# Optimization experiments

Hardware: AMD Instinct MI355X
Metric: run time of the kernel (lower is better)

The kernel has to match this reference:

```python
import jax, jax.numpy as jnp
import numpy as np
import math

B, S, D, H, DFF, E, TOPK = 2, 2048, 768, 12, 3072, 8, 2
DH = D // H
EPS = 1e-5


def _ln(x, g, b):
    mu = jnp.mean(x, axis=-1, keepdims=True)
    var = jnp.mean(jnp.square(x - mu), axis=-1, keepdims=True)
    return (x - mu) * jax.lax.rsqrt(var + EPS) * g + b


def _router(x, rw, rb):
    # x: [B,S,D] -> probs [B,S,E], topk indices [B,S,K]
    logits = jnp.einsum('bsd,de->bse', x, rw) + rb
    probs = jax.nn.softmax(logits, axis=-1)
    topv, topi = jax.lax.top_k(probs, TOPK)
    return probs, topv, topi


def setup_inputs() -> dict:
    key = jax.random.key(0)
    ks = jax.random.split(key, 12)
    s = 0.02
    inp = {
        'x': jax.random.normal(ks[0], (B, S, D), dtype=jnp.float32),
        'wq': jax.random.normal(ks[1], (D, D), dtype=jnp.float32) * s,
        'bq': jnp.zeros((D,), jnp.float32),
        'wk': jax.random.normal(ks[2], (D, D), dtype=jnp.float32) * s,
        'bk': jnp.zeros((D,), jnp.float32),
        'wv': jax.random.normal(ks[3], (D, D), dtype=jnp.float32) * s,
        'bv': jnp.zeros((D,), jnp.float32),
        'wo': jax.random.normal(ks[4], (D, D), dtype=jnp.float32) * s,
        'bo': jnp.zeros((D,), jnp.float32),
        'norm1_g': jnp.ones((D,), jnp.float32),
        'norm1_b': jnp.zeros((D,), jnp.float32),
        'router_w': jax.random.normal(ks[5], (D, E), dtype=jnp.float32) * s,
        'router_b': jnp.zeros((E,), jnp.float32),
        'ew1': jax.random.normal(ks[6], (E, D, DFF), dtype=jnp.float32) * s,
        'eb1': jnp.zeros((E, DFF), jnp.float32),
        'ew2': jax.random.normal(ks[7], (E, DFF, D), dtype=jnp.float32) * s,
        'eb2': jnp.zeros((E, D), jnp.float32),
        'norm2_g': jnp.ones((D,), jnp.float32),
        'norm2_b': jnp.zeros((D,), jnp.float32),
    }
    return inp


def reference(x, wq, bq, wk, bk, wv, bv, wo, bo,
              norm1_g, norm1_b, router_w, router_b,
              ew1, eb1, ew2, eb2, norm2_g, norm2_b):
    # ---- multi-head self-attention ----
    def proj(w, b):
        return (jnp.einsum('bsd,de->bse', x, w) + b).reshape(B, S, H, DH).transpose(0, 2, 1, 3)
    q, k, v = proj(wq, bq), proj(wk, bk), proj(wv, bv)
    scores = jnp.einsum('bhqd,bhkd->bhqk', q, k) / math.sqrt(DH)
    attn = jax.nn.softmax(scores, axis=-1)
    ctx = jnp.einsum('bhqk,bhkd->bhqd', attn, v).transpose(0, 2, 1, 3).reshape(B, S, D)
    attn_out = jnp.einsum('bsd,de->bse', ctx, wo) + bo
    x1 = _ln(x + attn_out, norm1_g, norm1_b)

    # ---- MoE: top-k routing with renormalized gates ----
    probs, topv, topi = _router(x1, router_w, router_b)
    gates = topv / jnp.sum(topv, axis=-1, keepdims=True)          # [B,S,K]
    # combine weights per expert: [B,S,E]
    combine = jnp.sum(jax.nn.one_hot(topi, E, dtype=x1.dtype) * gates[..., None], axis=-2)
    moe_out = jnp.zeros_like(x1)
    for e in range(E):  # fixed small expert count
        h = jax.nn.relu(jnp.einsum('bsd,df->bsf', x1, ew1[e]) + eb1[e])
        y = jnp.einsum('bsf,fd->bsd', h, ew2[e]) + eb2[e]
        moe_out = moe_out + combine[..., e:e + 1] * y
    x2 = _ln(x1 + moe_out, norm2_g, norm2_b)

    # ---- redundant second router call + load-balancing aux loss ----
    probs2, _, topi2 = _router(x2, router_w, router_b)
    mask2 = jax.nn.one_hot(topi2, E, dtype=x2.dtype)              # [B,S,K,E]
    frac = jnp.mean(mask2, axis=(0, 1, 2))                        # fraction routed per expert
    prob = jnp.mean(probs2, axis=(0, 1))                          # mean router prob per expert
    aux_loss = E * jnp.sum(frac * prob)
    return (x2, aux_loss)
```

## Files before the change

kernel.cpp:

```cpp
#include <hip/hip_runtime.h>

typedef _Float16 f16;
typedef _Float16 f16x8 __attribute__((ext_vector_type(8)));
typedef _Float16 f16x4v __attribute__((ext_vector_type(4)));
typedef float f32x4 __attribute__((ext_vector_type(4)));

#define THREADS 256
#define BM 128
#define BN 128
#define BKK 64

#define WSCALE 256.0f
#define WDESCALE (1.0f/256.0f)

static __device__ __forceinline__ float wred_sum(float x){
#pragma unroll
  for (int o = 32; o; o >>= 1) x += __shfl_xor(x, o);
  return x;
}
static __device__ __forceinline__ int wred_sumi(int x){
#pragma unroll
  for (int o = 32; o; o >>= 1) x += __shfl_xor(x, o);
  return x;
}
static __device__ __forceinline__ float bred_sum(float x){
  __shared__ float r[4];
  x = wred_sum(x);
  if ((threadIdx.x & 63) == 0) r[threadIdx.x >> 6] = x;
  __syncthreads();
  float s = r[0] + r[1] + r[2] + r[3];
  __syncthreads();
  return s;
}

template<class Epi>
static __device__ __forceinline__ void gemm_core(const f16* A, const f16* BT,
                                                 int m0, int K, int N, int n0, Epi epi)
{
  __shared__ __align__(16) f16 Al[BM][BKK];
  __shared__ __align__(16) f16 Bl[BN][BKK];
  const int t = threadIdx.x;
  const int lane = t & 63, wave = t >> 6;
  const int wr = wave >> 1, wc = wave & 1;

  const f16* gA[4];
  const f16* gB[4];
#pragma unroll
  for (int i = 0; i < 4; ++i) {
    int c = i * THREADS + t;
    int r = c >> 3;
    int kc = (((c & 7) ^ (r & 7)) << 3);
    gA[i] = A + (size_t)(m0 + r) * K + kc;
    gB[i] = BT + (size_t)(n0 + r) * K + kc;
  }

  f32x4 acc[4][4];
#pragma unroll
  for (int i = 0; i < 4; ++i)
#pragma unroll
    for (int j = 0; j < 4; ++j)
#pragma unroll
      for (int r = 0; r < 4; ++r) acc[i][j][r] = 0.0f;

  f16* Als = &Al[0][0];
  f16* Bls = &Bl[0][0];

  for (int k0 = 0; k0 < K; k0 += BKK) {
    __syncthreads();
#pragma unroll
    for (int i = 0; i < 4; ++i) {
      int c = i * THREADS + t;
      __builtin_amdgcn_global_load_lds(
          (const __attribute__((address_space(1))) void*)(gA[i] + k0),
          (__attribute__((address_space(3))) void*)(Als + (size_t)c * 8), 16, 0, 0);
      __builtin_amdgcn_global_load_lds(
          (const __attribute__((address_space(1))) void*)(gB[i] + k0),
          (__attribute__((address_space(3))) void*)(Bls + (size_t)c * 8), 16, 0, 0);
    }
    __syncthreads();
#pragma unroll
    for (int kk = 0; kk < BKK; kk += 32) {
      const int lrow = lane & 15, lk = (lane >> 4) * 8;
      const int sx = (lrow & 7) << 3;
      f16x8 af[4], bf[4];
#pragma unroll
      for (int mf = 0; mf < 4; ++mf)
        af[mf] = *(const f16x8*)&Als[(size_t)(wr * 64 + mf * 16 + lrow) * BKK + ((kk + lk) ^ sx)];
#pragma unroll
      for (int nf = 0; nf < 4; ++nf)
        bf[nf] = *(const f16x8*)&Bls[(size_t)(wc * 64 + nf * 16 + lrow) * BKK + ((kk + lk) ^ sx)];
#pragma unroll
      for (int mf = 0; mf < 4; ++mf)
#pragma unroll
        for (int nf = 0; nf < 4; ++nf)
          acc[mf][nf] = __builtin_amdgcn_mfma_f32_16x16x32_f16(af[mf], bf[nf], acc[mf][nf], 0, 0, 0);
    }
  }
  const int lr4 = (lane >> 4) * 4, lc = lane & 15;
#pragma unroll
  for (int mf = 0; mf < 4; ++mf)
#pragma unroll
    for (int nf = 0; nf < 4; ++nf)
#pragma unroll
      for (int r = 0; r < 4; ++r) {
        int row = wr * 64 + mf * 16 + lr4 + r;
        int col = n0 + wc * 64 + nf * 16 + lc;
        epi(row, col, acc[mf][nf][r]);
      }
}

__global__ __launch_bounds__(256) void k_cvt(const float* x, f16* o){
  size_t i = (size_t)blockIdx.x * 256 + threadIdx.x;
  float4 v = ((const float4*)x)[i];
  f16x4v h;
  h[0] = (f16)v.x; h[1] = (f16)v.y; h[2] = (f16)v.z; h[3] = (f16)v.w;
  *(f16x4v*)(o + i * 4) = h;
}

__global__ __launch_bounds__(256) void k_transpose(const float* in, f16* out, int Kd, int Nd){
  __shared__ float tl[32][33];
  const float* ip = in + (size_t)blockIdx.z * Kd * Nd;
  f16* op = out + (size_t)blockIdx.z * Kd * Nd;
  int n0 = blockIdx.x * 32, k0 = blockIdx.y * 32;
  int tx = threadIdx.x & 31, ty = threadIdx.x >> 5;
#pragma unroll
  for (int j = 0; j < 32; j += 8) tl[ty + j][tx] = ip[(size_t)(k0 + ty + j) * Nd + n0 + tx];
  __syncthreads();
#pragma unroll
  for (int j = 0; j < 32; j += 8) op[(size_t)(n0 + ty + j) * Kd + k0 + tx] = (f16)(tl[tx][ty + j] * WSCALE);
}

__global__ __launch_bounds__(256) void k_gemm_qkv(const f16* xb,
    const f16* wqT, const f16* wkT, const f16* wvT,
    const float* bq, const float* bk, const float* bv,
    f16* Q, f16* Ko, f16* V)
{
  int m0 = blockIdx.x * 128, n0 = blockIdx.y * 128, z = blockIdx.z;
  const f16* BT = (z == 0) ? wqT : ((z == 1) ? wkT : wvT);
  const float* bias = (z == 0) ? bq : ((z == 1) ? bk : bv);
  auto epi = [&](int row, int col, float vv) {
    int grow = m0 + row;
    int b = grow >> 11, s = grow & 2047;
    int h = col >> 6, dh = col & 63;
    float val = vv * WDESCALE + bias[col];
    if (z == 2) V[(((size_t)b * 12 + h) * 64 + dh) * 2048 + s] = (f16)val;
    else ((z == 0) ? Q : Ko)[(((size_t)b * 12 + h) * 2048 + s) * 64 + dh] = (f16)val;
  };
  gemm_core(xb, BT, m0, 768, 768, n0, epi);
}

__global__ __launch_bounds__(256, 4) void k_fattn(const f16* Qf, const f16* Kf,
                                                  const f16* Vf, float* Opart, float* lpart)
{
  __shared__ __align__(16) f16 Kl[64][72];
  __shared__ __align__(16) f16 Vl[64][72];
  __shared__ __align__(16) f16 Pl[64][72];
  const int t = threadIdx.x, lane = t & 63, wid = t >> 6;
  const int lc = lane & 15, g = lane >> 4;
  const int q0 = blockIdx.x * 64, bh = blockIdx.y, sp = blockIdx.z;
  const f16* Qh = Qf + (size_t)bh * 2048 * 64;
  const f16* Kh = Kf + ((size_t)bh * 2048 + sp * 1024) * 64;
  const f16* Vh = Vf + (size_t)bh * 64 * 2048 + sp * 1024;

  const float C1 = 0.125f * 1.44269504f;
  const float C2 = 9.0f - 2.0f * 1.44269504f;

  f16x8 aq[2];
#pragma unroll
  for (int kk = 0; kk < 2; ++kk)
    aq[kk] = *(const f16x8*)(Qh + (size_t)(q0 + wid * 16 + lc) * 64 + kk * 32 + g * 8);

  f32x4 acco[4];
  float l_[4];
#pragma unroll
  for (int nf = 0; nf < 4; ++nf)
#pragma unroll
    for (int r = 0; r < 4; ++r) acco[nf][r] = 0.f;
#pragma unroll
  for (int r = 0; r < 4; ++r) l_[r] = 0.f;

  f16x8 sk[2], sv[2];
#pragma unroll
  for (int i = 0; i < 2; ++i) {
    int c = i * 256 + t;
    sk[i] = *(const f16x8*)(Kh + (size_t)(c >> 3) * 64 + (c & 7) * 8);
    sv[i] = *(const f16x8*)(Vh + (size_t)(c >> 3) * 2048 + (c & 7) * 8);
  }

  for (int j = 0; j < 16; ++j) {
    __syncthreads();
#pragma unroll
    for (int i = 0; i < 2; ++i) {
      int c = i * 256 + t;
      *(f16x8*)&Kl[c >> 3][(c & 7) * 8] = sk[i];
      *(f16x8*)&Vl[c >> 3][(c & 7) * 8] = sv[i];
    }
    __syncthreads();

    if (j < 15) {
      const int kv1 = (j + 1) * 64;
#pragma unroll
      for (int i = 0; i < 2; ++i) {
        int c = i * 256 + t;
        sk[i] = *(const f16x8*)(Kh + (size_t)(kv1 + (c >> 3)) * 64 + (c & 7) * 8);
        sv[i] = *(const f16x8*)(Vh + (size_t)(c >> 3) * 2048 + kv1 + (c & 7) * 8);
      }
    }

    f32x4 acc[4];
#pragma unroll
    for (int nf = 0; nf < 4; ++nf)
#pragma unroll
      for (int r = 0; r < 4; ++r) acc[nf][r] = 0.f;
#pragma unroll
    for (int kk = 0; kk < 2; ++kk) {
      f16x8 bk[4];
#pragma unroll
      for (int nf = 0; nf < 4; ++nf) bk[nf] = *(const f16x8*)&Kl[nf * 16 + lc][kk * 32 + g * 8];
#pragma unroll
      for (int nf = 0; nf < 4; ++nf)
        acc[nf] = __builtin_amdgcn_mfma_f32_16x16x32_f16(aq[kk], bk[nf], acc[nf], 0, 0, 0);
    }

    {
      const int prow = wid * 16 + g * 4;
#pragma unroll
      for (int r = 0; r < 4; ++r) {
        float ls = 0.f;
#pragma unroll
        for (int nf = 0; nf < 4; ++nf) {
          float p = exp2f(fmaf(acc[nf][r], C1, C2));
          Pl[prow + r][nf * 16 + lc] = (f16)p;
          ls += p;
        }
        l_[r] += ls;
      }
    }

#pragma unroll
    for (int kk = 0; kk < 2; ++kk) {
      f16x8 ap, bv[4];
      ap = *(const f16x8*)&Pl[wid * 16 + lc][kk * 32 + g * 8];
#pragma unroll
      for (int nf = 0; nf < 4; ++nf) bv[nf] = *(const f16x8*)&Vl[nf * 16 + lc][kk * 32 + g * 8];
#pragma unroll
      for (int nf = 0; nf < 4; ++nf)
        acco[nf] = __builtin_amdgcn_mfma_f32_16x16x32_f16(ap, bv[nf], acco[nf], 0, 0, 0);
    }
  }

  float* Op = Opart + ((size_t)(sp * 24 + bh) * 2048 + q0) * 64;
  float* lp = lpart + (size_t)(sp * 24 + bh) * 2048 + q0;
#pragma unroll
  for (int r = 0; r < 4; ++r) {
    float lr = l_[r];
#pragma unroll
    for (int o = 1; o < 16; o <<= 1) lr += __shfl_xor(lr, o);
    if (lc == 0) lp[wid * 16 + g * 4 + r] = lr;
#pragma unroll
    for (int nf = 0; nf < 4; ++nf)
      Op[(size_t)(wid * 16 + g * 4 + r) * 64 + nf * 16 + lc] = acco[nf][r];
  }
}

__global__ __launch_bounds__(256) void k_attcomb(const float* Opart, const float* lpart, f16* ctx){
  size_t base = ((size_t)blockIdx.x * 256 + threadIdx.x) * 4;
  size_t row = base >> 6; int dh = base & 63;
  int bh = (int)(row >> 11), qr = (int)(row & 2047);
  int b = bh / 12, h = bh - b * 12;
  const float4 o0 = *(const float4*)(Opart + base);
  const float4 o1 = *(const float4*)(Opart + base + (size_t)24 * 2048 * 64);
  float inv = 1.f / (lpart[row] + lpart[row + 24 * 2048]);
  f16x4v hv;
  hv[0] = (f16)((o0.x + o1.x) * inv);
  hv[1] = (f16)((o0.y + o1.y) * inv);
  hv[2] = (f16)((o0.z + o1.z) * inv);
  hv[3] = (f16)((o0.w + o1.w) * inv);
  *(f16x4v*)(ctx + ((size_t)b * 2048 + qr) * 768 + h * 64 + dh) = hv;
}

__global__ __launch_bounds__(256) void k_gemm_oproj(const f16* ctx, const f16* woT,
    const float* bo, const float* x, float* x1pre)
{
  int m0 = blockIdx.x * 128, n0 = blockIdx.y * 128;
  auto epi = [&](int row, int col, float vv) {
    size_t i = (size_t)(m0 + row) * 768 + col;
    x1pre[i] = x[i] + vv * WDESCALE + bo[col];
  };
  gemm_core(ctx, woT, m0, 768, 768, n0, epi);
}

__global__ __launch_bounds__(256) void k_ln(const float* in, const float* add,
    const float* g, const float* b, float* outf, f16* outh)
{
  size_t row = blockIdx.x;
  int t = threadIdx.x;
  const float* p = in + row * 768;
  float v[3];
  float s = 0.f;
#pragma unroll
  for (int i = 0; i < 3; ++i) {
    float xv = p[t + i * 256];
    if (add) xv += add[row * 768 + t + i * 256];
    v[i] = xv; s += xv;
  }
  float mu = bred_sum(s) * (1.f / 768.f);
  float q = 0.f;
#pragma unroll
  for (int i = 0; i < 3; ++i) { float d = v[i] - mu; q += d * d; }
  float var = bred_sum(q) * (1.f / 768.f);
  float inv = rsqrtf(var + 1e-5f);
#pragma unroll
  for (int i = 0; i < 3; ++i) {
    int c = t + i * 256;
    float y = (v[i] - mu) * inv * g[c] + b[c];
    outf[row * 768 + c] = y;
    if (outh) outh[row * 768 + c] = (f16)y;
  }
}

__global__ __launch_bounds__(256) void k_ln_moe(const float* x1, const f16* ys,
    const int* inv_map, const float* gates, const float* g, const float* b, float* outf)
{
  size_t row = blockIdx.x;
  int t = threadIdx.x;
  int sl0 = inv_map[row * 2], sl1 = inv_map[row * 2 + 1];
  float g0 = gates[row * 2], g1 = gates[row * 2 + 1];
  const float* p = x1 + row * 768;
  const f16* y0 = ys + (size_t)sl0 * 768;
  const f16* y1 = ys + (size_t)sl1 * 768;
  float v[3];
  float s = 0.f;
#pragma unroll
  for (int i = 0; i < 3; ++i) {
    int c = t + i * 256;
    float xv = p[c] + g0 * (float)y0[c] + g1 * (float)y1[c];
    v[i] = xv; s += xv;
  }
  float mu = bred_sum(s) * (1.f / 768.f);
  float q = 0.f;
#pragma unroll
  for (int i = 0; i < 3; ++i) { float d = v[i] - mu; q += d * d; }
  float var = bred_sum(q) * (1.f / 768.f);
  float inv = rsqrtf(var + 1e-5f);
#pragma unroll
  for (int i = 0; i < 3; ++i) {
    int c = t + i * 256;
    outf[row * 768 + c] = (v[i] - mu) * inv * g[c] + b[c];
  }
}

__global__ __launch_bounds__(256) void k_router(const float* X, const float* rw, const float* rb,
    int* topi, float* gates, float* pprob_part, int* pcnt_part, int mode)
{
  __shared__ float sp[4][8];
  __shared__ int   si[4][2];
  int wave = threadIdx.x >> 6;
  int tok = blockIdx.x * 4 + wave;
  int lane = threadIdx.x & 63;
  const float* xr = X + (size_t)tok * 768;
  float a0=0,a1=0,a2=0,a3=0,a4=0,a5=0,a6=0,a7=0;
#pragma unroll
  for (int i = 0; i < 12; ++i) {
    int d = lane + i * 64;
    float xv = xr[d];
    float4 w0 = *(const float4*)(rw + d * 8);
    float4 w1 = *(const float4*)(rw + d * 8 + 4);
    a0 += xv*w0.x; a1 += xv*w0.y; a2 += xv*w0.z; a3 += xv*w0.w;
    a4 += xv*w1.x; a5 += xv*w1.y; a6 += xv*w1.z; a7 += xv*w1.w;
  }
  a0=wred_sum(a0); a1=wred_sum(a1); a2=wred_sum(a2); a3=wred_sum(a3);
  a4=wred_sum(a4); a5=wred_sum(a5); a6=wred_sum(a6); a7=wred_sum(a7);
  if (lane == 0) {
    float lg[8] = {a0+rb[0],a1+rb[1],a2+rb[2],a3+rb[3],a4+rb[4],a5+rb[5],a6+rb[6],a7+rb[7]};
    float mx = lg[0];
    for (int e = 1; e < 8; ++e) mx = fmaxf(mx, lg[e]);
    float pp[8], ssum = 0.f;
    for (int e = 0; e < 8; ++e) { pp[e] = expf(lg[e] - mx); ssum += pp[e]; }
    float invs = 1.f / ssum;
    for (int e = 0; e < 8; ++e) pp[e] *= invs;
    int i1 = 0; float p1 = pp[0];
    for (int e = 1; e < 8; ++e) if (pp[e] > p1) { p1 = pp[e]; i1 = e; }
    int i2 = -1; float p2 = -1.f;
    for (int e = 0; e < 8; ++e) if (e != i1 && pp[e] > p2) { p2 = pp[e]; i2 = e; }
    if (mode == 1) {
      float gs = 1.f / (p1 + p2);
      topi[tok*2] = i1; topi[tok*2+1] = i2;
      gates[tok*2] = p1*gs; gates[tok*2+1] = p2*gs;
    } else {
      for (int e = 0; e < 8; ++e) sp[wave][e] = pp[e];
      si[wave][0] = i1; si[wave][1] = i2;
    }
  }
  if (mode == 2) {
    __syncthreads();
    int t = threadIdx.x;
    if (t < 8) {
      float s = sp[0][t] + sp[1][t] + sp[2][t] + sp[3][t];
      int c = 0;
#pragma unroll
      for (int w = 0; w < 4; ++w) c += (si[w][0] == t) + (si[w][1] == t);
      pprob_part[blockIdx.x * 8 + t] = s;
      pcnt_part[blockIdx.x * 8 + t] = c;
    }
  }
}

__global__ __launch_bounds__(256) void k_plan(const int* topi, int* offal,
    int* tile_e, int* tile_r0, int* tile_e2, int* tile_r02)
{
  __shared__ int hist[8];
  int t = threadIdx.x, lane = t & 63;
  if (t < 8) hist[t] = 0;
  __syncthreads();
  int loc[8] = {0,0,0,0,0,0,0,0};
  for (int i = t; i < 8192; i += 256) ++loc[topi[i]];
#pragma unroll
  for (int e = 0; e < 8; ++e) {
    int s = wred_sumi(loc[e]);
    if (lane == 0) atomicAdd(&hist[e], s);
  }
  __syncthreads();
  if (t == 0) {
    int off = 0, t1 = 0, t2 = 0;
    for (int e = 0; e < 8; ++e) {
      offal[e] = off;
      int nt = (hist[e] + 255) >> 8;
      for (int i = 0; i < nt; ++i) {
        tile_e[t1] = e; tile_r0[t1] = off + i * 256; ++t1;
        tile_e2[t2] = e; tile_r02[t2] = off + i * 256; ++t2;
        tile_e2[t2] = e; tile_r02[t2] = off + i * 256 + 128; ++t2;
      }
      off += nt << 8;
    }
    for (; t1 < 40; ++t1) { tile_e[t1] = -1; tile_r0[t1] = 0; }
    for (; t2 < 80; ++t2) { tile_e2[t2] = -1; tile_r02[t2] = 0; }
  }
}

__global__ __launch_bounds__(512) void k_scatter(const int* topi, const float* gates,
    const int* offal, int* perm, float* gate_s, int* inv_map)
{
  int w = threadIdx.x >> 6, lane = threadIdx.x & 63;
  int base = offal[w];
  for (int it = 0; it < 128; ++it) {
    int i = it * 64 + lane;
    int e = topi[i];
    bool act = (e == w);
    unsigned long long mask = __ballot(act);
    if (act) {
      int pos = base + __popcll(mask & ((1ull << lane) - 1ull));
      perm[pos] = i >> 1;
      gate_s[pos] = gates[i];
      inv_map[i] = pos;
    }
    base += __popcll(mask);
  }
}

__global__ __launch_bounds__(512, 1) void k_gemm_moe1(const f16* x1b, const f16* ew1T,
    const float* eb1, const int* tile_e, const int* tile_r0, const int* perm, f16* hbuf)
{
  __shared__ __align__(16) f16 Al[2][256][64];
  __shared__ __align__(16) f16 Bl[2][256][64];
  int e = tile_e[blockIdx.x];
  if (e < 0) return;
  int s0 = tile_r0[blockIdx.x];
  int n0 = blockIdx.y * 256;
  const f16* BT = ew1T + (size_t)e * 3072 * 768 + (size_t)n0 * 768;
  const float* be = eb1 + e * 3072;

  const int t = threadIdx.x;
  const int lane = t & 63, wave = t >> 6;
  const int wr = wave >> 2, wc = wave & 3;

  const f16* gA[4];
  const f16* gB[4];
#pragma unroll
  for (int i = 0; i < 4; ++i) {
    int c = i * 512 + t;
    int r = c >> 3;
    int kc = (((c & 7) ^ (r & 7)) << 3);
    gA[i] = x1b + (size_t)perm[s0 + r] * 768 + kc;
    gB[i] = BT + (size_t)r * 768 + kc;
  }

  f32x4 acc[8][4];
#pragma unroll
  for (int i = 0; i < 8; ++i)
#pragma unroll
    for (int j = 0; j < 4; ++j)
#pragma unroll
      for (int r = 0; r < 4; ++r) acc[i][j][r] = 0.0f;

  auto stage = [&](int buf, int k0) {
    f16* Ad = &Al[buf][0][0];
    f16* Bd = &Bl[buf][0][0];
#pragma unroll
    for (int i = 0; i < 4; ++i) {
      int c = i * 512 + t;
      __builtin_amdgcn_global_load_lds(
          (const __attribute__((address_space(1))) void*)(gA[i] + k0),
          (__attribute__((address_space(3))) void*)(Ad + (size_t)c * 8), 16, 0, 0);
      __builtin_amdgcn_global_load_lds(
          (const __attribute__((address_space(1))) void*)(gB[i] + k0),
          (__attribute__((address_space(3))) void*)(Bd + (size_t)c * 8), 16, 0, 0);
    }
  };

  stage(0, 0);
  stage(1, 64);

  for (int ks = 0; ks < 12; ++ks) {
    const int cur = ks & 1;
    if (ks < 11) asm volatile("s_waitcnt vmcnt(8)" ::: "memory");
    else         asm volatile("s_waitcnt vmcnt(0)" ::: "memory");
    __builtin_amdgcn_s_barrier();
    asm volatile("" ::: "memory");

    const f16* Ab = &Al[cur][0][0];
    const f16* Bb = &Bl[cur][0][0];
#pragma unroll
    for (int kk = 0; kk < 64; kk += 32) {
      const int lrow = lane & 15, lk = (lane >> 4) * 8;
      const int sx = (lrow & 7) << 3;
      f16x8 af[8], bf[4];
#pragma unroll
      for (int mf = 0; mf < 8; ++mf)
        af[mf] = *(const f16x8*)&Ab[(size_t)(wr * 128 + mf * 16 + lrow) * 64 + ((kk + lk) ^ sx)];
#pragma unroll
      for (int nf = 0; nf < 4; ++nf)
        bf[nf] = *(const f16x8*)&Bb[(size_t)(wc * 64 + nf * 16 + lrow) * 64 + ((kk + lk) ^ sx)];
#pragma unroll
      for (int mf = 0; mf < 8; ++mf)
#pragma unroll
        for (int nf = 0; nf < 4; ++nf)
          acc[mf][nf] = __builtin_amdgcn_mfma_f32_16x16x32_f16(af[mf], bf[nf], acc[mf][nf], 0, 0, 0);
    }

    asm volatile("" ::: "memory");
    __builtin_amdgcn_s_barrier();
    asm volatile("" ::: "memory");
    if (ks < 10) stage(cur, (ks + 2) * 64);
  }

  const int lr4 = (lane >> 4) * 4, lc = lane & 15;
#pragma unroll
  for (int mf = 0; mf < 8; ++mf)
#pragma unroll
    for (int nf = 0; nf < 4; ++nf)
#pragma unroll
      for (int r = 0; r < 4; ++r) {
        int row = wr * 128 + mf * 16 + lr4 + r;
        int col = n0 + wc * 64 + nf * 16 + lc;
        hbuf[(size_t)(s0 + row) * 3072 + col] = (f16)fmaxf(acc[mf][nf][r] * WDESCALE + be[col], 0.f);
      }
}

__global__ __launch_bounds__(256) void k_gemm_moe2(const f16* hbuf, const f16* ew2T,
    const float* eb2, const int* tile_e2, const int* tile_r02, f16* yslots)
{
  int e = tile_e2[blockIdx.x];
  if (e < 0) return;
  int s0 = tile_r02[blockIdx.x];
  int n0 = blockIdx.y * 128;
  const f16* A = hbuf + (size_t)s0 * 3072;
  const f16* BT = ew2T + (size_t)e * 768 * 3072;
  const float* be = eb2 + e * 768;
  auto epi = [&](int row, int col, float vv) {
    yslots[(size_t)(s0 + row) * 768 + col] = (f16)(vv * WDESCALE + be[col]);
  };
  gemm_core(A, BT, 0, 3072, 768, n0, epi);
}

__global__ __launch_bounds__(256) void k_final(const float* pprob, const int* pcnt, float* out){
  __shared__ float sp[256];
  __shared__ int sc[256];
  int t = threadIdx.x, e = t & 7, g = t >> 3;
  float s = 0.f; int c = 0;
  for (int b = g; b < 1024; b += 32) { s += pprob[b * 8 + e]; c += pcnt[b * 8 + e]; }
  sp[t] = s; sc[t] = c;
  __syncthreads();
  if (t < 8) {
    float ss = 0.f; int cc = 0;
    for (int g2 = 0; g2 < 32; ++g2) { ss += sp[t + g2 * 8]; cc += sc[t + g2 * 8]; }
    sp[t] = ss; sc[t] = cc;
  }
  __syncthreads();
  if (t == 0) {
    float a = 0.f;
    for (int e2 = 0; e2 < 8; ++e2)
      a += ((float)sc[e2] * (1.f / 8192.f)) * (sp[e2] * (1.f / 4096.f));
    out[(size_t)4096 * 768] = 8.f * a;
  }
}

extern "C" void kernel_launch(void* const* d_in, const int* in_sizes, int n_in,
                              void* d_out, int out_size, void* d_ws, size_t ws_size,
                              hipStream_t stream)
{
  const float* x   = (const float*)d_in[0];
  const float* wq  = (const float*)d_in[1];
  const float* bq  = (const float*)d_in[2];
  const float* wk  = (const float*)d_in[3];
  const float* bk  = (const float*)d_in[4];
  const float* wv  = (const float*)d_in[5];
  const float* bv  = (const float*)d_in[6];
  const float* wo  = (const float*)d_in[7];
  const float* bo  = (const float*)d_in[8];
  const float* n1g = (const float*)d_in[9];
  const float* n1b = (const float*)d_in[10];
  const float* rw  = (const float*)d_in[11];
  const float* rb  = (const float*)d_in[12];
  const float* ew1 = (const float*)d_in[13];
  const float* eb1 = (const float*)d_in[14];
  const float* ew2 = (const float*)d_in[15];
  const float* eb2 = (const float*)d_in[16];
  const float* n2g = (const float*)d_in[17];
  const float* n2b = (const float*)d_in[18];
  float* out = (float*)d_out;
  char* ws = (char*)d_ws;

  size_t oWQT,oWKT,oWVT,oWOT,oEW1T,oEW2T,oXB,oQ,oK,oV,oCTX,oX1,oX1B,oYS;
  size_t oTOPI,oGATES,oOFF,oTE,oTR,oTE2,oTR2,oPERM,oGS,oINV,oH,oPP,oPC,oOP,oLP;

  {
    size_t off = 0;
    auto al = [&](size_t bytes) { size_t o = off; off += (bytes + 255) & ~(size_t)255; return o; };
    oWQT = al((size_t)768*768*2); oWKT = al((size_t)768*768*2);
    oWVT = al((size_t)768*768*2); oWOT = al((size_t)768*768*2);
    oEW1T = al((size_t)8*768*3072*2); oEW2T = al((size_t)8*768*3072*2);
    oXB  = al((size_t)4096*768*2);
    oQ   = al((size_t)24*2048*64*2); oK = al((size_t)24*2048*64*2); oV = al((size_t)24*2048*64*2);
    oCTX = al((size_t)4096*768*2);
    oX1  = al((size_t)4096*768*4);
    oX1B = al((size_t)4096*768*2);
    oYS  = al((size_t)10240*768*2);
    oTOPI = al(4096*2*4); oGATES = al(4096*2*4);
    oOFF = al(256);
    oTE = al(256); oTR = al(256); oTE2 = al(512); oTR2 = al(512);
    oPERM = al(10240*4); oGS = al(10240*4); oINV = al(8192*4);
    oH = al((size_t)10240*3072*2);
    oPP = al(1024*8*4); oPC = al(1024*8*4);
    oOP = al((size_t)2*24*2048*64*4);
    oLP = al((size_t)2*24*2048*4);
    (void)ws_size;
  }

  f16* wqT  = (f16*)(ws + oWQT);
  f16* wkT  = (f16*)(ws + oWKT);
  f16* wvT  = (f16*)(ws + oWVT);
  f16* woT  = (f16*)(ws + oWOT);
  f16* ew1T = (f16*)(ws + oEW1T);
  f16* ew2T = (f16*)(ws + oEW2T);
  f16* xb   = (f16*)(ws + oXB);
  f16* Qf   = (f16*)(ws + oQ);
  f16* Kf   = (f16*)(ws + oK);
  f16* Vf   = (f16*)(ws + oV);
  f16* ctxb = (f16*)(ws + oCTX);
  float* x1 = (float*)(ws + oX1);
  f16* x1bb = (f16*)(ws + oX1B);
  f16* yslots = (f16*)(ws + oYS);
  int* topi = (int*)(ws + oTOPI);
  float* gates = (float*)(ws + oGATES);
  int* offal  = (int*)(ws + oOFF);
  int* tile_e = (int*)(ws + oTE);
  int* tile_r0= (int*)(ws + oTR);
  int* tile_e2 = (int*)(ws + oTE2);
  int* tile_r02= (int*)(ws + oTR2);
  int* perm   = (int*)(ws + oPERM);
  float* gate_s = (float*)(ws + oGS);
  int* inv_map = (int*)(ws + oINV);
  f16* hbuf   = (f16*)(ws + oH);
  float* pprob = (float*)(ws + oPP);
  int* pcnt   = (int*)(ws + oPC);
  float* Opart = (float*)(ws + oOP);
  float* lpart = (float*)(ws + oLP);

  (void)in_sizes; (void)n_in; (void)out_size;

  hipMemsetAsync(ws + oPERM, 0, 2 * 10240 * 4, stream);

  k_cvt<<<3072, 256, 0, stream>>>(x, xb);
  k_transpose<<<dim3(24,24,1), 256, 0, stream>>>(wq, wqT, 768, 768);
  k_transpose<<<dim3(24,24,1), 256, 0, stream>>>(wk, wkT, 768, 768);
  k_transpose<<<dim3(24,24,1), 256, 0, stream>>>(wv, wvT, 768, 768);
  k_transpose<<<dim3(24,24,1), 256, 0, stream>>>(wo, woT, 768, 768);
  k_transpose<<<dim3(96,24,8), 256, 0, stream>>>(ew1, ew1T, 768, 3072);
  k_transpose<<<dim3(24,96,8), 256, 0, stream>>>(ew2, ew2T, 3072, 768);

  k_gemm_qkv<<<dim3(32,6,3), 256, 0, stream>>>(xb, wqT, wkT, wvT, bq, bk, bv, Qf, Kf, Vf);
  k_fattn<<<dim3(32,24,2), 256, 0, stream>>>(Qf, Kf, Vf, Opart, lpart);
  k_attcomb<<<3072, 256, 0, stream>>>(Opart, lpart, ctxb);
  k_gemm_oproj<<<dim3(32,6), 256, 0, stream>>>(ctxb, woT, bo, x, x1);
  k_ln<<<4096, 256, 0, stream>>>(x1, nullptr, n1g, n1b, x1, x1bb);

  k_router<<<1024, 256, 0, stream>>>(x1, rw, rb, topi, gates, pprob, pcnt, 1);
  k_plan<<<1, 256, 0, stream>>>(topi, offal, tile_e, tile_r0, tile_e2, tile_r02);
  k_scatter<<<1, 512, 0, stream>>>(topi, gates, offal, perm, gate_s, inv_map);
  k_gemm_moe1<<<dim3(40,12), 512, 0, stream>>>(x1bb, ew1T, eb1, tile_e, tile_r0, perm, hbuf);
  k_gemm_moe2<<<dim3(80,6), 256, 0, stream>>>(hbuf, ew2T, eb2, tile_e2, tile_r02, yslots);

  k_ln_moe<<<4096, 256, 0, stream>>>(x1, yslots, inv_map, gates, n2g, n2b, out);
  k_router<<<1024, 256, 0, stream>>>(out, rw, rb, topi, gates, pprob, pcnt, 2);
  k_final<<<1, 256, 0, stream>>>(pprob, pcnt, out);
}
```

Before: 438.3 us.

## Rewrite MoE down-projection GEMM with 128x256 tiles and triple-buffered direct-to-LDS loads

```diff
diff --git a/kernel.cpp b/kernel.cpp
--- a/kernel.cpp
+++ b/kernel.cpp
@@ -557,20 +557,131 @@
       }
 }
 
-__global__ __launch_bounds__(256) void k_gemm_moe2(const f16* hbuf, const f16* ew2T,
+__global__ __launch_bounds__(512, 1) void k_gemm_moe2(const f16* hbuf, const f16* ew2T,
     const float* eb2, const int* tile_e2, const int* tile_r02, f16* yslots)
 {
+  __shared__ __align__(16) f16 Al[3][128][64];
+  __shared__ __align__(16) f16 Bl[3][256][64];
   int e = tile_e2[blockIdx.x];
   if (e < 0) return;
   int s0 = tile_r02[blockIdx.x];
-  int n0 = blockIdx.y * 128;
-  const f16* A = hbuf + (size_t)s0 * 3072;
-  const f16* BT = ew2T + (size_t)e * 768 * 3072;
+  int n0 = blockIdx.y * 256;
+  const f16* A  = hbuf + (size_t)s0 * 3072;
+  const f16* BT = ew2T + (size_t)e * 768 * 3072 + (size_t)n0 * 3072;
   const float* be = eb2 + e * 768;
-  auto epi = [&](int row, int col, float vv) {
-    yslots[(size_t)(s0 + row) * 768 + col] = (f16)(vv * WDESCALE + be[col]);
+
+  const int t = threadIdx.x;
+  const int lane = t & 63, wave = t >> 6;
+  const int wr = wave >> 2, wc = wave & 3;
+
+  const f16* gA[2];
+  const f16* gB[4];
+#pragma unroll
+  for (int i = 0; i < 2; ++i) {
+    int c = i * 512 + t;
+    int r = c >> 3;
+    int kc = (((c & 7) ^ (r & 7)) << 3);
+    gA[i] = A + (size_t)r * 3072 + kc;
+  }
+#pragma unroll
+  for (int i = 0; i < 4; ++i) {
+    int c = i * 512 + t;
+    int r = c >> 3;
+    int kc = (((c & 7) ^ (r & 7)) << 3);
+    gB[i] = BT + (size_t)r * 3072 + kc;
+  }
+
+  f32x4 acc[4][4];
+#pragma unroll
+  for (int i = 0; i < 4; ++i)
+#pragma unroll
+    for (int j = 0; j < 4; ++j)
+#pragma unroll
+      for (int r = 0; r < 4; ++r) acc[i][j][r] = 0.0f;
+
+  auto stage = [&](int buf, int k0) {
+    f16* Ad = &Al[buf][0][0];
+    f16* Bd = &Bl[buf][0][0];
+#pragma unroll
+    for (int i = 0; i < 2; ++i) {
+      int c = i * 512 + t;
+      __builtin_amdgcn_global_load_lds(
+          (const __attribute__((address_space(1))) void*)(gA[i] + k0),
+          (__attribute__((address_space(3))) void*)(Ad + (size_t)c * 8), 16, 0, 0);
+    }
+#pragma unroll
+    for (int i = 0; i < 4; ++i) {
+      int c = i * 512 + t;
+      __builtin_amdgcn_global_load_lds(
+          (const __attribute__((address_space(1))) void*)(gB[i] + k0),
+          (__attribute__((address_space(3))) void*)(Bd + (size_t)c * 8), 16, 0, 0);
+    }
   };
-  gemm_core(A, BT, 0, 3072, 768, n0, epi);
+
+  stage(0, 0);
+  stage(1, 64);
+
+  int bufc = 0;
+  for (int ks = 0; ks < 48; ++ks) {
+    if (ks < 47) asm volatile("s_waitcnt vmcnt(6)" ::: "memory");
+    else         asm volatile("s_waitcnt vmcnt(0)" ::: "memory");
+    __builtin_amdgcn_s_barrier();
+    asm volatile("" ::: "memory");
+
+    const f16* Ab = &Al[bufc][0][0];
+    const f16* Bb = &Bl[bufc][0][0];
+    const int lrow = lane & 15, lk = (lane >> 4) * 8;
+    const int sx = (lrow & 7) << 3;
+
+    {
+      f16x8 af[4], bf[4];
+#pragma unroll
+      for (int mf = 0; mf < 4; ++mf)
+        af[mf] = *(const f16x8*)&Ab[(size_t)(wr * 64 + mf * 16 + lrow) * 64 + ((0 + lk) ^ sx)];
+#pragma unroll
+      for (int nf = 0; nf < 4; ++nf)
+        bf[nf] = *(const f16x8*)&Bb[(size_t)(wc * 64 + nf * 16 + lrow) * 64 + ((0 + lk) ^ sx)];
+#pragma unroll
+      for (int mf = 0; mf < 4; ++mf)
+#pragma unroll
+        for (int nf = 0; nf < 4; ++nf)
+          acc[mf][nf] = __builtin_amdgcn_mfma_f32_16x16x32_f16(af[mf], bf[nf], acc[mf][nf], 0, 0, 0);
+    }
+
+    if (ks < 46) {
+      int nb = bufc + 2; if (nb >= 3) nb -= 3;
+      stage(nb, (ks + 2) * 64);
+    }
+
+    {
+      f16x8 af[4], bf[4];
+#pragma unroll
+      for (int mf = 0; mf < 4; ++mf)
+        af[mf] = *(const f16x8*)&Ab[(size_t)(wr * 64 + mf * 16 + lrow) * 64 + ((32 + lk) ^ sx)];
+#pragma unroll
+      for (int nf = 0; nf < 4; ++nf)
+        bf[nf] = *(const f16x8*)&Bb[(size_t)(wc * 64 + nf * 16 + lrow) * 64 + ((32 + lk) ^ sx)];
+#pragma unroll
+      for (int mf = 0; mf < 4; ++mf)
+#pragma unroll
+        for (int nf = 0; nf < 4; ++nf)
+          acc[mf][nf] = __builtin_amdgcn_mfma_f32_16x16x32_f16(af[mf], bf[nf], acc[mf][nf], 0, 0, 0);
+    }
+
+    ++bufc; if (bufc >= 3) bufc = 0;
+  }
+
+  const int lr4 = (lane >> 4) * 4, lc = lane & 15;
+#pragma unroll
+  for (int mf = 0; mf < 4; ++mf)
+#pragma unroll
+    for (int nf = 0; nf < 4; ++nf)
+#pragma unroll
+      for (int r = 0; r < 4; ++r) {
+        int row = wr * 64 + mf * 16 + lr4 + r;
+        int col = n0 + wc * 64 + nf * 16 + lc;
+        yslots[(size_t)(s0 + row) * 768 + col] = (f16)(acc[mf][nf][r] * WDESCALE + be[col]);
+      }
 }
 
 __global__ __launch_bounds__(256) void k_final(const float* pprob, const int* pcnt, float* out){
@@ -699,7 +810,7 @@
   k_plan<<<1, 256, 0, stream>>>(topi, offal, tile_e, tile_r0, tile_e2, tile_r02);
   k_scatter<<<1, 512, 0, stream>>>(topi, gates, offal, perm, gate_s, inv_map);
   k_gemm_moe1<<<dim3(40,12), 512, 0, stream>>>(x1bb, ew1T, eb1, tile_e, tile_r0, perm, hbuf);
-  k_gemm_moe2<<<dim3(80,6), 256, 0, stream>>>(hbuf, ew2T, eb2, tile_e2, tile_r02, yslots);
+  k_gemm_moe2<<<dim3(80,3), 512, 0, stream>>>(hbuf, ew2T, eb2, tile_e2, tile_r02, yslots);
 
   k_ln_moe<<<4096, 256, 0, stream>>>(x1, yslots, inv_map, gates, n2g, n2b, out);
   k_router<<<1024, 256, 0, stream>>>(out, rw, rb, topi, gates, pprob, pcnt, 2);
```

Result: slower. 452.5 us (+3.3%).
